# Kernel optimization log

Hardware: AMD Instinct MI355X
Metric: run time of the kernel (lower is better)

The kernel has to match this reference:

```python
import jax, jax.numpy as jnp
import numpy as np

N_Q, N_KV, DIM, D_K, D_V = 4096, 4096, 1024, 1024, 1024

def setup_inputs() -> dict:
    key = jax.random.key(0)
    ks = jax.random.split(key, 6)
    return {
        "q": jax.random.normal(ks[0], (N_Q, DIM), dtype=jnp.float32),
        "k": jax.random.normal(ks[1], (N_KV, DIM), dtype=jnp.float32),
        "v": jax.random.normal(ks[2], (N_KV, DIM), dtype=jnp.float32),
        "W_q": jax.random.uniform(ks[3], (DIM, D_K), dtype=jnp.float32),
        "W_k": jax.random.uniform(ks[4], (DIM, D_V), dtype=jnp.float32),
        "W_v": jax.random.uniform(ks[5], (DIM, D_V), dtype=jnp.float32),
    }

def reference(q, k, v, W_q, W_k, W_v) -> jnp.ndarray:
    d_k = W_q.shape[1]
    Q = q @ W_q                      # (n, d_k)
    K = k @ W_k                      # (N, d_v)
    V = v @ W_v                      # (N, d_v)
    scores = (Q @ K.T) / jnp.sqrt(jnp.asarray(d_k, Q.dtype))  # (n, N)
    attn = jax.nn.softmax(scores, axis=-1)
    return attn @ V                  # (n, d_v)
```

## Files before the change

kernel.cpp:

```cpp
#include <hip/hip_runtime.h>
#include <hip/hip_bf16.h>
#include <stdint.h>

typedef float  f32x4  __attribute__((ext_vector_type(4)));
typedef short  s16x8  __attribute__((ext_vector_type(8)));
typedef unsigned short u16;

#define BK 32

__device__ inline u16 f32_to_bf16_rn(float f) {
  uint32_t u = __builtin_bit_cast(uint32_t, f);
  u += 0x7FFFu + ((u >> 16) & 1u);
  return (u16)(u >> 16);
}
__device__ inline float bf16u_to_f32(u16 h) {
  uint32_t u = ((uint32_t)h) << 16;
  return __builtin_bit_cast(float, u);
}
__device__ inline void split2(float x, u16& hi, u16& lo) {
  u16 h = f32_to_bf16_rn(x);
  lo = f32_to_bf16_rn(x - bf16u_to_f32(h));
  hi = h;
}

__device__ inline void stage16(const u16* g, const u16* l) {
  __builtin_amdgcn_global_load_lds((const __attribute__((address_space(1))) uint32_t*)g,
                                   (__attribute__((address_space(3))) uint32_t*)(u16*)l,
                                   16, 0, 0);
}

__device__ inline void xcd_swz(int& bx, int& by) {
  int nx = gridDim.x, nwg = nx * gridDim.y;
  if ((nwg & 7) == 0) {
    int wg = blockIdx.x + nx * blockIdx.y;
    int s = (wg & 7) * (nwg >> 3) + (wg >> 3);
    bx = s % nx;
    by = s / nx;
  } else {
    bx = blockIdx.x;
    by = blockIdx.y;
  }
}


__global__ __launch_bounds__(256) void split_rows3(const float* __restrict__ in0,
                                                   const float* __restrict__ in1,
                                                   const float* __restrict__ in2,
                                                   u16* __restrict__ hi0, u16* __restrict__ lo0,
                                                   u16* __restrict__ hi1, u16* __restrict__ lo1,
                                                   u16* __restrict__ hi2, u16* __restrict__ lo2,
                                                   int n4) {
  int i = blockIdx.x * 256 + threadIdx.x;
  if (i >= n4) return;
  const float* in = blockIdx.z == 0 ? in0 : blockIdx.z == 1 ? in1 : in2;
  u16* hi = blockIdx.z == 0 ? hi0 : blockIdx.z == 1 ? hi1 : hi2;
  u16* lo = blockIdx.z == 0 ? lo0 : blockIdx.z == 1 ? lo1 : lo2;
  float4 t = ((const float4*)in)[i];
  ushort4 h, l;
  split2(t.x, h.x, l.x);
  split2(t.y, h.y, l.y);
  split2(t.z, h.z, l.z);
  split2(t.w, h.w, l.w);
  ((ushort4*)hi)[i] = h;
  ((ushort4*)lo)[i] = l;
}

__global__ __launch_bounds__(256) void split_transpose3(const float* __restrict__ in0,
                                                        const float* __restrict__ in1,
                                                        const float* __restrict__ in2,
                                                        u16* __restrict__ thi0, u16* __restrict__ tlo0,
                                                        u16* __restrict__ thi1, u16* __restrict__ tlo1,
                                                        u16* __restrict__ thi2, u16* __restrict__ tlo2,
                                                        int R, int C) {
  const float* in = blockIdx.z == 0 ? in0 : blockIdx.z == 1 ? in1 : in2;
  u16* thi = blockIdx.z == 0 ? thi0 : blockIdx.z == 1 ? thi1 : thi2;
  u16* tlo = blockIdx.z == 0 ? tlo0 : blockIdx.z == 1 ? tlo1 : tlo2;
  __shared__ float tile[32][33];
  int tx = threadIdx.x & 31, ty = threadIdx.x >> 5;
  int r0 = blockIdx.y * 32, c0 = blockIdx.x * 32;
#pragma unroll
  for (int j = 0; j < 32; j += 8)
    tile[ty + j][tx] = in[(size_t)(r0 + ty + j) * C + c0 + tx];
  __syncthreads();
#pragma unroll
  for (int j = 0; j < 32; j += 8) {
    float x = tile[tx][ty + j];
    u16 h, l;
    split2(x, h, l);
    size_t o = (size_t)(c0 + ty + j) * R + r0 + tx;
    thi[o] = h;
    tlo[o] = l;
  }
}

__global__ __launch_bounds__(256) void transpose_u16_2(const u16* __restrict__ in0,
                                                       const u16* __restrict__ in1,
                                                       u16* __restrict__ out0,
                                                       u16* __restrict__ out1, int R, int C) {
  const u16* in = blockIdx.z == 0 ? in0 : in1;
  u16* out = blockIdx.z == 0 ? out0 : out1;
  __shared__ u16 tile[32][33];
  int tx = threadIdx.x & 31, ty = threadIdx.x >> 5;
  int r0 = blockIdx.y * 32, c0 = blockIdx.x * 32;
#pragma unroll
  for (int j = 0; j < 32; j += 8)
    tile[ty + j][tx] = in[(size_t)(r0 + ty + j) * C + c0 + tx];
  __syncthreads();
#pragma unroll
  for (int j = 0; j < 32; j += 8)
    out[(size_t)(c0 + ty + j) * R + r0 + tx] = tile[tx][ty + j];
}

__global__ __launch_bounds__(256) void add_inplace(float* __restrict__ a,
                                                   const float* __restrict__ b, int n4) {
  int i = blockIdx.x * 256 + threadIdx.x;
  if (i >= n4) return;
  float4 x = ((const float4*)a)[i];
  float4 y = ((const float4*)b)[i];
  x.x += y.x; x.y += y.y; x.z += y.z; x.w += y.w;
  ((float4*)a)[i] = x;
}

template <int TBN, int OUT_SPLIT>
__device__ __forceinline__ void gemm8p_body(
    const u16* __restrict__ Ahi, const u16* __restrict__ Alo, int lda,
    const u16* __restrict__ Bhi, const u16* __restrict__ Blo, int ldb,
    float* __restrict__ Cf, u16* __restrict__ Chi, u16* __restrict__ Clo, int ldc,
    int NT, int k0, float scale, int arow0, int bcol0) {
  constexpr int NW = TBN / 4;
  constexpr int FN = NW / 16;
  constexpr int NCA = 256 * 8;
  constexpr int NCB = TBN * 8;
  constexpr int TISS = (NCA + NCB) / 512;
  constexpr int H1 = (TISS + 1) / 2;
  constexpr int BB = NCA * 8;

  __shared__ alignas(16) u16 lds[2][(NCA + NCB) * 8];

  const int tid = threadIdx.x;
  const int lane = tid & 63;
  const int wid = tid >> 6;
  const int wr = wid >> 2;
  const int wc = wid & 3;
  const int frow = lane & 15;
  const int koct = lane >> 4;

  const u16* src[TISS];
  int loff[TISS];
#pragma unroll
  for (int j = 0; j < TISS; ++j) {
    int g = j * 512 + wid * 64 + lane;
    loff[j] = g * 8;
    if (g < NCA) {
      int r = g >> 3, ch = g & 7, c2 = ch ^ (r & 7);
      const u16* base = (c2 < 4) ? Ahi : Alo;
      src[j] = base + (size_t)(arow0 + r) * lda + k0 + (c2 & 3) * 8;
    } else {
      int gb = g - NCA;
      int r = gb >> 3, ch = gb & 7, c2 = ch ^ (r & 7);
      const u16* base = (c2 < 4) ? Bhi : Blo;
      src[j] = base + (size_t)(bcol0 + r) * ldb + k0 + (c2 & 3) * 8;
    }
  }

  f32x4 acc[8][FN];
#pragma unroll
  for (int m = 0; m < 8; ++m)
#pragma unroll
    for (int n = 0; n < FN; ++n) acc[m][n] = (f32x4)0.0f;

#pragma unroll
  for (int j = 0; j < TISS; ++j) stage16(src[j], &lds[0][loff[j]]);
#pragma unroll
  for (int j = 0; j < TISS; ++j) src[j] += BK;
  asm volatile("s_waitcnt vmcnt(0)" ::: "memory");
  __builtin_amdgcn_sched_barrier(0);
  __builtin_amdgcn_s_barrier();

  for (int t = 0; t < NT; ++t) {
    const u16* cur = lds[t & 1];
    const u16* nxt = lds[(t + 1) & 1];
    const bool st = (t + 1 < NT);
    s16x8 bh[FN], bl[FN];
#pragma unroll
    for (int p = 0; p < 4; ++p) {
      s16x8 ah[2], al[2];
      if (p == 0) {
#pragma unroll
        for (int n = 0; n < FN; ++n) {
          int br = wc * NW + n * 16 + frow;
          bh[n] = *(const s16x8*)&cur[BB + br * 64 + ((koct ^ (br & 7)) << 3)];
          bl[n] = *(const s16x8*)&cur[BB + br * 64 + (((4 | koct) ^ (br & 7)) << 3)];
        }
      }
#pragma unroll
      for (int m = 0; m < 2; ++m) {
        int ar = wr * 128 + p * 32 + m * 16 + frow;
        ah[m] = *(const s16x8*)&cur[ar * 64 + ((koct ^ (ar & 7)) << 3)];
        al[m] = *(const s16x8*)&cur[ar * 64 + (((4 | koct) ^ (ar & 7)) << 3)];
      }
      if (st && p == 0) {
#pragma unroll
        for (int j = 0; j < H1; ++j) stage16(src[j], &nxt[loff[j]]);
      }
      if (st && p == 1) {
#pragma unroll
        for (int j = H1; j < TISS; ++j) stage16(src[j], &nxt[loff[j]]);
#pragma unroll
        for (int j = 0; j < TISS; ++j) src[j] += BK;
      }
      __builtin_amdgcn_sched_barrier(0);
      __builtin_amdgcn_s_barrier();
      asm volatile("s_waitcnt lgkmcnt(0)" ::: "memory");
      __builtin_amdgcn_sched_barrier(0);
      __builtin_amdgcn_s_setprio(1);
#pragma unroll
      for (int m = 0; m < 2; ++m)
#pragma unroll
        for (int n = 0; n < FN; ++n) {
          acc[p * 2 + m][n] =
              __builtin_amdgcn_mfma_f32_16x16x32_bf16(ah[m], bh[n], acc[p * 2 + m][n], 0, 0, 0);
          acc[p * 2 + m][n] =
              __builtin_amdgcn_mfma_f32_16x16x32_bf16(ah[m], bl[n], acc[p * 2 + m][n], 0, 0, 0);
          acc[p * 2 + m][n] =
              __builtin_amdgcn_mfma_f32_16x16x32_bf16(al[m], bh[n], acc[p * 2 + m][n], 0, 0, 0);
        }
      __builtin_amdgcn_s_setprio(0);
      __builtin_amdgcn_sched_barrier(0);
      if (p == 3) {
        asm volatile("s_waitcnt vmcnt(0)" ::: "memory");
        __builtin_amdgcn_sched_barrier(0);
      }
      __builtin_amdgcn_s_barrier();
    }
  }

  const int rb = arow0 + wr * 128 + koct * 4;
  const int cb = bcol0 + wc * NW + frow;
#pragma unroll
  for (int mg = 0; mg < 8; ++mg)
#pragma unroll
    for (int n = 0; n < FN; ++n)
#pragma unroll
      for (int r = 0; r < 4; ++r) {
        int row = rb + mg * 16 + r;
        int col = cb + n * 16;
        float val = acc[mg][n][r] * scale;
        if (OUT_SPLIT) {
          u16 h, l;
          split2(val, h, l);
          Chi[(size_t)row * ldc + col] = h;
          Clo[(size_t)row * ldc + col] = l;
        } else {
          Cf[(size_t)row * ldc + col] = val;
        }
      }
}

__global__ __launch_bounds__(512, 2) void scores8p(
    const u16* __restrict__ Ahi, const u16* __restrict__ Alo, int lda,
    const u16* __restrict__ Bhi, const u16* __restrict__ Blo, int ldb,
    float* __restrict__ Cf, int ldc, int NT, float scale) {
  int bx, by;
  xcd_swz(bx, by);
  gemm8p_body<256, 0>(Ahi, Alo, lda, Bhi, Blo, ldb, Cf, nullptr, nullptr, ldc,
                      NT, 0, scale, by * 256, bx * 256);
}

__global__ __launch_bounds__(512, 2) void proj8p(
    const u16* __restrict__ a0h, const u16* __restrict__ a0l,
    const u16* __restrict__ a1h, const u16* __restrict__ a1l,
    const u16* __restrict__ a2h, const u16* __restrict__ a2l,
    const u16* __restrict__ b0h, const u16* __restrict__ b0l,
    const u16* __restrict__ b1h, const u16* __restrict__ b1l,
    const u16* __restrict__ b2h, const u16* __restrict__ b2l,
    u16* __restrict__ c0h, u16* __restrict__ c0l,
    u16* __restrict__ c1h, u16* __restrict__ c1l,
    u16* __restrict__ c2h, u16* __restrict__ c2l,
    int D, float scale0) {
  const int z = blockIdx.z;
  const u16* Ah = z == 0 ? a0h : z == 1 ? a1h : a2h;
  const u16* Al = z == 0 ? a0l : z == 1 ? a1l : a2l;
  const u16* Bh = z == 0 ? b0h : z == 1 ? b1h : b2h;
  const u16* Bl = z == 0 ? b0l : z == 1 ? b1l : b2l;
  u16* Ch = z == 0 ? c0h : z == 1 ? c1h : c2h;
  u16* Cl = z == 0 ? c0l : z == 1 ? c1l : c2l;
  float scale = z == 0 ? scale0 : 1.0f;
  int bx, by;
  xcd_swz(bx, by);
  gemm8p_body<128, 1>(Ah, Al, D, Bh, Bl, D, nullptr, Ch, Cl, D,
                      D / BK, 0, scale, by * 256, bx * 128);
}

__global__ __launch_bounds__(512, 2) void pv8p(
    const u16* __restrict__ Ahi, const u16* __restrict__ Alo, int lda,
    const u16* __restrict__ Bhi, const u16* __restrict__ Blo, int ldb,
    float* __restrict__ Cf0, float* __restrict__ Cf1, int ldc, int KH) {
  float* Cf = blockIdx.z == 0 ? Cf0 : Cf1;
  int bx, by;
  xcd_swz(bx, by);
  gemm8p_body<128, 0>(Ahi, Alo, lda, Bhi, Blo, ldb, Cf, nullptr, nullptr, ldc,
                      KH / BK, blockIdx.z * KH, 1.0f, by * 256, bx * 128);
}

__global__ __launch_bounds__(256) void softmax_rows(float* __restrict__ S, int N) {
  const int tid = threadIdx.x;
  float* row = S + (size_t)blockIdx.x * N;
  const float4* row4 = (const float4*)row;
  float v[16];
#pragma unroll
  for (int i = 0; i < 4; ++i) {
    float4 t = row4[tid + i * 256];
    v[i * 4 + 0] = t.x;
    v[i * 4 + 1] = t.y;
    v[i * 4 + 2] = t.z;
    v[i * 4 + 3] = t.w;
  }
  float m = -__builtin_inff();
#pragma unroll
  for (int i = 0; i < 16; ++i) m = fmaxf(m, v[i]);
#pragma unroll
  for (int o = 32; o > 0; o >>= 1) m = fmaxf(m, __shfl_xor(m, o));
  __shared__ float redm[4];
  __shared__ float reds[4];
  const int wid = tid >> 6;
  if ((tid & 63) == 0) redm[wid] = m;
  __syncthreads();
  m = fmaxf(fmaxf(redm[0], redm[1]), fmaxf(redm[2], redm[3]));

  float s = 0.f;
#pragma unroll
  for (int i = 0; i < 16; ++i) {
    v[i] = __expf(v[i] - m);
    s += v[i];
  }
#pragma unroll
  for (int o = 32; o > 0; o >>= 1) s += __shfl_xor(s, o);
  if ((tid & 63) == 0) reds[wid] = s;
  __syncthreads();
  s = reds[0] + reds[1] + reds[2] + reds[3];
  float inv = 1.0f / s;

  u16* hrow = (u16*)row;
  u16* lrow = hrow + N;
#pragma unroll
  for (int i = 0; i < 4; ++i) {
    ushort4 h4, l4;
    split2(v[i * 4 + 0] * inv, h4.x, l4.x);
    split2(v[i * 4 + 1] * inv, h4.y, l4.y);
    split2(v[i * 4 + 2] * inv, h4.z, l4.z);
    split2(v[i * 4 + 3] * inv, h4.w, l4.w);
    ((ushort4*)hrow)[tid + i * 256] = h4;
    ((ushort4*)lrow)[tid + i * 256] = l4;
  }
}

extern "C" void kernel_launch(void* const* d_in, const int* in_sizes, int n_in,
                              void* d_out, int out_size, void* d_ws, size_t ws_size,
                              hipStream_t stream) {
  (void)in_sizes; (void)n_in; (void)out_size; (void)ws_size;
  const float* q  = (const float*)d_in[0];
  const float* k  = (const float*)d_in[1];
  const float* v  = (const float*)d_in[2];
  const float* Wq = (const float*)d_in[3];
  const float* Wk = (const float*)d_in[4];
  const float* Wv = (const float*)d_in[5];
  float* out = (float*)d_out;

  char* ws = (char*)d_ws;
  const size_t MB = 1ull << 20;
  u16* q_hi = (u16*)(ws + 0 * MB);
  u16* q_lo = (u16*)(ws + 8 * MB);
  u16* k_hi = (u16*)(ws + 16 * MB);
  u16* k_lo = (u16*)(ws + 24 * MB);
  u16* v_hi = (u16*)(ws + 32 * MB);
  u16* v_lo = (u16*)(ws + 40 * MB);
  u16* V_hi = (u16*)(ws + 48 * MB);
  u16* V_lo = (u16*)(ws + 56 * MB);
  float* S  = (float*)(ws + 0 * MB);
  u16* WqT_hi = (u16*)(ws + 64 * MB);
  u16* WqT_lo = (u16*)(ws + 66 * MB);
  u16* WkT_hi = (u16*)(ws + 68 * MB);
  u16* WkT_lo = (u16*)(ws + 70 * MB);
  u16* WvT_hi = (u16*)(ws + 72 * MB);
  u16* WvT_lo = (u16*)(ws + 74 * MB);
  u16* Q_hi = (u16*)(ws + 76 * MB);
  u16* Q_lo = (u16*)(ws + 84 * MB);
  u16* K_hi = (u16*)(ws + 92 * MB);
  u16* K_lo = (u16*)(ws + 100 * MB);
  u16* VT_hi = (u16*)(ws + 108 * MB);
  u16* VT_lo = (u16*)(ws + 116 * MB);
  float* PVp1 = (float*)(ws + 76 * MB);

  const int NQ = 4096, NKV = 4096, D = 1024;

  int n4 = NQ * D / 4;
  split_rows3<<<dim3(n4 / 256, 1, 3), 256, 0, stream>>>(q, k, v, q_hi, q_lo, k_hi, k_lo,
                                                        v_hi, v_lo, n4);

  split_transpose3<<<dim3(D / 32, D / 32, 3), 256, 0, stream>>>(
      Wq, Wk, Wv, WqT_hi, WqT_lo, WkT_hi, WkT_lo, WvT_hi, WvT_lo, D, D);

  proj8p<<<dim3(D / 128, NQ / 256, 3), 512, 0, stream>>>(
      q_hi, q_lo, k_hi, k_lo, v_hi, v_lo,
      WqT_hi, WqT_lo, WkT_hi, WkT_lo, WvT_hi, WvT_lo,
      Q_hi, Q_lo, K_hi, K_lo, V_hi, V_lo, D, 0.03125f);

  transpose_u16_2<<<dim3(D / 32, NKV / 32, 2), 256, 0, stream>>>(V_hi, V_lo, VT_hi, VT_lo,
                                                                 NKV, D);

  scores8p<<<dim3(NKV / 256, NQ / 256), 512, 0, stream>>>(Q_hi, Q_lo, D, K_hi, K_lo, D,
                                                          S, NKV, D / BK, 1.0f);

  softmax_rows<<<NQ, 256, 0, stream>>>(S, NKV);

  pv8p<<<dim3(D / 128, NQ / 256, 2), 512, 0, stream>>>(
      (u16*)S, (u16*)S + NKV, 2 * NKV, VT_hi, VT_lo, NKV, out, PVp1, D, NKV / 2);

  add_inplace<<<NQ * D / 4 / 256, 256, 0, stream>>>(out, PVp1, NQ * D / 4);
}
```

Baseline: 405.5 us.

## Triple-buffer GEMM LDS pipeline and shrink scores tile to 256x128

The shared GEMM body goes from double to triple buffering in LDS, prefetching two K-steps ahead and using partial vmcnt waits so global loads overlap more compute. The scores kernel also drops from 256x256 to 256x128 tiles, doubling its grid, and the body is fixed at a 128-wide N tile. Three 48KB buffers raise LDS use to 144KB per block, which may cut the two-blocks-per-CU occupancy the launch bounds request. The scores tile change lowers operand reuse per block.

```diff
diff --git a/kernel.cpp b/kernel.cpp
--- a/kernel.cpp
+++ b/kernel.cpp
@@ -121,21 +121,20 @@
   ((float4*)a)[i] = x;
 }
 
-template <int TBN, int OUT_SPLIT>
-__device__ __forceinline__ void gemm8p_body(
+template <int OUT_SPLIT>
+__device__ __forceinline__ void gemm3b_body(
     const u16* __restrict__ Ahi, const u16* __restrict__ Alo, int lda,
     const u16* __restrict__ Bhi, const u16* __restrict__ Blo, int ldb,
     float* __restrict__ Cf, u16* __restrict__ Chi, u16* __restrict__ Clo, int ldc,
     int NT, int k0, float scale, int arow0, int bcol0) {
-  constexpr int NW = TBN / 4;
-  constexpr int FN = NW / 16;
   constexpr int NCA = 256 * 8;
-  constexpr int NCB = TBN * 8;
+  constexpr int NCB = 128 * 8;
   constexpr int TISS = (NCA + NCB) / 512;
-  constexpr int H1 = (TISS + 1) / 2;
+  constexpr int H1 = TISS / 2;
   constexpr int BB = NCA * 8;
-
-  __shared__ alignas(16) u16 lds[2][(NCA + NCB) * 8];
+  constexpr int BUFSZ = (NCA + NCB) * 8;
+
+  __shared__ alignas(16) u16 lds[3][BUFSZ];
 
   const int tid = threadIdx.x;
   const int lane = tid & 63;
@@ -163,32 +162,40 @@
     }
   }
 
-  f32x4 acc[8][FN];
+  f32x4 acc[8][2];
 #pragma unroll
   for (int m = 0; m < 8; ++m)
 #pragma unroll
-    for (int n = 0; n < FN; ++n) acc[m][n] = (f32x4)0.0f;
+    for (int n = 0; n < 2; ++n) acc[m][n] = (f32x4)0.0f;
 
 #pragma unroll
   for (int j = 0; j < TISS; ++j) stage16(src[j], &lds[0][loff[j]]);
 #pragma unroll
   for (int j = 0; j < TISS; ++j) src[j] += BK;
-  asm volatile("s_waitcnt vmcnt(0)" ::: "memory");
+  if (NT > 1) {
+#pragma unroll
+    for (int j = 0; j < TISS; ++j) stage16(src[j], &lds[1][loff[j]]);
+#pragma unroll
+    for (int j = 0; j < TISS; ++j) src[j] += BK;
+    asm volatile("s_waitcnt vmcnt(6)" ::: "memory");
+  } else {
+    asm volatile("s_waitcnt vmcnt(0)" ::: "memory");
+  }
   __builtin_amdgcn_sched_barrier(0);
   __builtin_amdgcn_s_barrier();
 
   for (int t = 0; t < NT; ++t) {
-    const u16* cur = lds[t & 1];
-    const u16* nxt = lds[(t + 1) & 1];
-    const bool st = (t + 1 < NT);
-    s16x8 bh[FN], bl[FN];
+    const u16* cur = lds[t % 3];
+    const u16* nx2 = lds[(t + 2) % 3];
+    const bool st = (t + 2 < NT);
+    s16x8 bh[2], bl[2];
 #pragma unroll
     for (int p = 0; p < 4; ++p) {
       s16x8 ah[2], al[2];
       if (p == 0) {
 #pragma unroll
-        for (int n = 0; n < FN; ++n) {
-          int br = wc * NW + n * 16 + frow;
+        for (int n = 0; n < 2; ++n) {
+          int br = wc * 32 + n * 16 + frow;
           bh[n] = *(const s16x8*)&cur[BB + br * 64 + ((koct ^ (br & 7)) << 3)];
           bl[n] = *(const s16x8*)&cur[BB + br * 64 + (((4 | koct) ^ (br & 7)) << 3)];
         }
@@ -201,11 +208,11 @@
       }
       if (st && p == 0) {
 #pragma unroll
-        for (int j = 0; j < H1; ++j) stage16(src[j], &nxt[loff[j]]);
+        for (int j = 0; j < H1; ++j) stage16(src[j], &nx2[loff[j]]);
       }
       if (st && p == 1) {
 #pragma unroll
-        for (int j = H1; j < TISS; ++j) stage16(src[j], &nxt[loff[j]]);
+        for (int j = H1; j < TISS; ++j) stage16(src[j], &nx2[loff[j]]);
 #pragma unroll
         for (int j = 0; j < TISS; ++j) src[j] += BK;
       }
@@ -217,7 +224,7 @@
 #pragma unroll
       for (int m = 0; m < 2; ++m)
 #pragma unroll
-        for (int n = 0; n < FN; ++n) {
+        for (int n = 0; n < 2; ++n) {
           acc[p * 2 + m][n] =
               __builtin_amdgcn_mfma_f32_16x16x32_bf16(ah[m], bh[n], acc[p * 2 + m][n], 0, 0, 0);
           acc[p * 2 + m][n] =
@@ -228,7 +235,11 @@
       __builtin_amdgcn_s_setprio(0);
       __builtin_amdgcn_sched_barrier(0);
       if (p == 3) {
-        asm volatile("s_waitcnt vmcnt(0)" ::: "memory");
+        if (st) {
+          asm volatile("s_waitcnt vmcnt(6)" ::: "memory");
+        } else {
+          asm volatile("s_waitcnt vmcnt(0)" ::: "memory");
+        }
         __builtin_amdgcn_sched_barrier(0);
       }
       __builtin_amdgcn_s_barrier();
@@ -236,11 +247,11 @@
   }
 
   const int rb = arow0 + wr * 128 + koct * 4;
-  const int cb = bcol0 + wc * NW + frow;
+  const int cb = bcol0 + wc * 32 + frow;
 #pragma unroll
   for (int mg = 0; mg < 8; ++mg)
 #pragma unroll
-    for (int n = 0; n < FN; ++n)
+    for (int n = 0; n < 2; ++n)
 #pragma unroll
       for (int r = 0; r < 4; ++r) {
         int row = rb + mg * 16 + r;
@@ -263,8 +274,8 @@
     float* __restrict__ Cf, int ldc, int NT, float scale) {
   int bx, by;
   xcd_swz(bx, by);
-  gemm8p_body<256, 0>(Ahi, Alo, lda, Bhi, Blo, ldb, Cf, nullptr, nullptr, ldc,
-                      NT, 0, scale, by * 256, bx * 256);
+  gemm3b_body<0>(Ahi, Alo, lda, Bhi, Blo, ldb, Cf, nullptr, nullptr, ldc,
+                 NT, 0, scale, by * 256, bx * 128);
 }
 
 __global__ __launch_bounds__(512, 2) void proj8p(
@@ -288,8 +299,8 @@
   float scale = z == 0 ? scale0 : 1.0f;
   int bx, by;
   xcd_swz(bx, by);
-  gemm8p_body<128, 1>(Ah, Al, D, Bh, Bl, D, nullptr, Ch, Cl, D,
-                      D / BK, 0, scale, by * 256, bx * 128);
+  gemm3b_body<1>(Ah, Al, D, Bh, Bl, D, nullptr, Ch, Cl, D,
+                 D / BK, 0, scale, by * 256, bx * 128);
 }
 
 __global__ __launch_bounds__(512, 2) void pv8p(
@@ -299,8 +310,8 @@
   float* Cf = blockIdx.z == 0 ? Cf0 : Cf1;
   int bx, by;
   xcd_swz(bx, by);
-  gemm8p_body<128, 0>(Ahi, Alo, lda, Bhi, Blo, ldb, Cf, nullptr, nullptr, ldc,
-                      KH / BK, blockIdx.z * KH, 1.0f, by * 256, bx * 128);
+  gemm3b_body<0>(Ahi, Alo, lda, Bhi, Blo, ldb, Cf, nullptr, nullptr, ldc,
+                 KH / BK, blockIdx.z * KH, 1.0f, by * 256, bx * 128);
 }
 
 __global__ __launch_bounds__(256) void softmax_rows(float* __restrict__ S, int N) {
@@ -409,7 +420,7 @@
   transpose_u16_2<<<dim3(D / 32, NKV / 32, 2), 256, 0, stream>>>(V_hi, V_lo, VT_hi, VT_lo,
                                                                  NKV, D);
 
-  scores8p<<<dim3(NKV / 256, NQ / 256), 512, 0, stream>>>(Q_hi, Q_lo, D, K_hi, K_lo, D,
+  scores8p<<<dim3(NKV / 128, NQ / 256), 512, 0, stream>>>(Q_hi, Q_lo, D, K_hi, K_lo, D,
                                                           S, NKV, D / BK, 1.0f);
 
   softmax_rows<<<NQ, 256, 0, stream>>>(S, NKV);
```

After: 431.7 us. 6.5% more time.

## Reorder GEMM tile staging for partial vmcnt waits and widen projection tiles

Applied to the files above, without the earlier changes.

The shared GEMM body now issues the B-tile loads first and then the A-tile loads in an interleaved order. It replaces the full vmcnt(0) drain with partial waits at phases 1 and 3, so the next tile's global loads can keep flowing while the current data is consumed. The projection kernel also moves from 256x128 to 256x256 tiles, which halves its grid and raises reuse per block but adds register pressure and cuts parallelism. The partial-wait counts rely on the exact order of issued loads, which adds a correctness risk.

```diff
diff --git a/kernel.cpp b/kernel.cpp
--- a/kernel.cpp
+++ b/kernel.cpp
@@ -122,17 +122,16 @@
 }
 
 template <int TBN, int OUT_SPLIT>
-__device__ __forceinline__ void gemm8p_body(
+__device__ __forceinline__ void gemm2c_body(
     const u16* __restrict__ Ahi, const u16* __restrict__ Alo, int lda,
     const u16* __restrict__ Bhi, const u16* __restrict__ Blo, int ldb,
     float* __restrict__ Cf, u16* __restrict__ Chi, u16* __restrict__ Clo, int ldc,
     int NT, int k0, float scale, int arow0, int bcol0) {
-  constexpr int NW = TBN / 4;
-  constexpr int FN = NW / 16;
-  constexpr int NCA = 256 * 8;
+  constexpr int NCA = 2048;
   constexpr int NCB = TBN * 8;
-  constexpr int TISS = (NCA + NCB) / 512;
-  constexpr int H1 = (TISS + 1) / 2;
+  constexpr int NBI = NCB / 512;
+  constexpr int TISS = NBI + 4;
+  constexpr int FN = TBN / 64;
   constexpr int BB = NCA * 8;
 
   __shared__ alignas(16) u16 lds[2][(NCA + NCB) * 8];
@@ -147,19 +146,21 @@
 
   const u16* src[TISS];
   int loff[TISS];
-#pragma unroll
-  for (int j = 0; j < TISS; ++j) {
-    int g = j * 512 + wid * 64 + lane;
-    loff[j] = g * 8;
-    if (g < NCA) {
+  const int aj[4] = {0, 2, 1, 3};
+#pragma unroll
+  for (int s = 0; s < TISS; ++s) {
+    if (s < NBI) {
+      int g = s * 512 + tid;
+      int r = g >> 3, ch = g & 7, c2 = ch ^ (r & 7);
+      const u16* base = (c2 < 4) ? Bhi : Blo;
+      src[s] = base + (size_t)(bcol0 + r) * ldb + k0 + (c2 & 3) * 8;
+      loff[s] = BB + g * 8;
+    } else {
+      int g = aj[s - NBI] * 512 + tid;
       int r = g >> 3, ch = g & 7, c2 = ch ^ (r & 7);
       const u16* base = (c2 < 4) ? Ahi : Alo;
-      src[j] = base + (size_t)(arow0 + r) * lda + k0 + (c2 & 3) * 8;
-    } else {
-      int gb = g - NCA;
-      int r = gb >> 3, ch = gb & 7, c2 = ch ^ (r & 7);
-      const u16* base = (c2 < 4) ? Bhi : Blo;
-      src[j] = base + (size_t)(bcol0 + r) * ldb + k0 + (c2 & 3) * 8;
+      src[s] = base + (size_t)(arow0 + r) * lda + k0 + (c2 & 3) * 8;
+      loff[s] = g * 8;
     }
   }
 
@@ -170,10 +171,10 @@
     for (int n = 0; n < FN; ++n) acc[m][n] = (f32x4)0.0f;
 
 #pragma unroll
-  for (int j = 0; j < TISS; ++j) stage16(src[j], &lds[0][loff[j]]);
-#pragma unroll
-  for (int j = 0; j < TISS; ++j) src[j] += BK;
-  asm volatile("s_waitcnt vmcnt(0)" ::: "memory");
+  for (int s = 0; s < TISS; ++s) stage16(src[s], &lds[0][loff[s]]);
+#pragma unroll
+  for (int s = 0; s < TISS; ++s) src[s] += BK;
+  asm volatile("s_waitcnt vmcnt(2)" ::: "memory");
   __builtin_amdgcn_sched_barrier(0);
   __builtin_amdgcn_s_barrier();
 
@@ -188,7 +189,7 @@
       if (p == 0) {
 #pragma unroll
         for (int n = 0; n < FN; ++n) {
-          int br = wc * NW + n * 16 + frow;
+          int br = wc * (TBN / 4) + n * 16 + frow;
           bh[n] = *(const s16x8*)&cur[BB + br * 64 + ((koct ^ (br & 7)) << 3)];
           bl[n] = *(const s16x8*)&cur[BB + br * 64 + (((4 | koct) ^ (br & 7)) << 3)];
         }
@@ -201,13 +202,13 @@
       }
       if (st && p == 0) {
 #pragma unroll
-        for (int j = 0; j < H1; ++j) stage16(src[j], &nxt[loff[j]]);
+        for (int s = 0; s < TISS - 2; ++s) stage16(src[s], &nxt[loff[s]]);
       }
       if (st && p == 1) {
 #pragma unroll
-        for (int j = H1; j < TISS; ++j) stage16(src[j], &nxt[loff[j]]);
-#pragma unroll
-        for (int j = 0; j < TISS; ++j) src[j] += BK;
+        for (int s = TISS - 2; s < TISS; ++s) stage16(src[s], &nxt[loff[s]]);
+#pragma unroll
+        for (int s = 0; s < TISS; ++s) src[s] += BK;
       }
       __builtin_amdgcn_sched_barrier(0);
       __builtin_amdgcn_s_barrier();
@@ -227,8 +228,16 @@
         }
       __builtin_amdgcn_s_setprio(0);
       __builtin_amdgcn_sched_barrier(0);
-      if (p == 3) {
-        asm volatile("s_waitcnt vmcnt(0)" ::: "memory");
+      if (p == 1) {
+        if (st) {
+          asm volatile("s_waitcnt vmcnt(%0)" ::"i"(TISS) : "memory");
+        } else {
+          asm volatile("s_waitcnt vmcnt(0)" ::: "memory");
+        }
+        __builtin_amdgcn_sched_barrier(0);
+      }
+      if (p == 3 && st) {
+        asm volatile("s_waitcnt vmcnt(2)" ::: "memory");
         __builtin_amdgcn_sched_barrier(0);
       }
       __builtin_amdgcn_s_barrier();
@@ -236,7 +245,7 @@
   }
 
   const int rb = arow0 + wr * 128 + koct * 4;
-  const int cb = bcol0 + wc * NW + frow;
+  const int cb = bcol0 + wc * (TBN / 4) + frow;
 #pragma unroll
   for (int mg = 0; mg < 8; ++mg)
 #pragma unroll
@@ -263,7 +272,7 @@
     float* __restrict__ Cf, int ldc, int NT, float scale) {
   int bx, by;
   xcd_swz(bx, by);
-  gemm8p_body<256, 0>(Ahi, Alo, lda, Bhi, Blo, ldb, Cf, nullptr, nullptr, ldc,
+  gemm2c_body<256, 0>(Ahi, Alo, lda, Bhi, Blo, ldb, Cf, nullptr, nullptr, ldc,
                       NT, 0, scale, by * 256, bx * 256);
 }
 
@@ -288,8 +297,8 @@
   float scale = z == 0 ? scale0 : 1.0f;
   int bx, by;
   xcd_swz(bx, by);
-  gemm8p_body<128, 1>(Ah, Al, D, Bh, Bl, D, nullptr, Ch, Cl, D,
-                      D / BK, 0, scale, by * 256, bx * 128);
+  gemm2c_body<256, 1>(Ah, Al, D, Bh, Bl, D, nullptr, Ch, Cl, D,
+                      D / BK, 0, scale, by * 256, bx * 256);
 }
 
 __global__ __launch_bounds__(512, 2) void pv8p(
@@ -299,7 +308,7 @@
   float* Cf = blockIdx.z == 0 ? Cf0 : Cf1;
   int bx, by;
   xcd_swz(bx, by);
-  gemm8p_body<128, 0>(Ahi, Alo, lda, Bhi, Blo, ldb, Cf, nullptr, nullptr, ldc,
+  gemm2c_body<128, 0>(Ahi, Alo, lda, Bhi, Blo, ldb, Cf, nullptr, nullptr, ldc,
                       KH / BK, blockIdx.z * KH, 1.0f, by * 256, bx * 128);
 }
 
@@ -401,7 +410,7 @@
   split_transpose3<<<dim3(D / 32, D / 32, 3), 256, 0, stream>>>(
       Wq, Wk, Wv, WqT_hi, WqT_lo, WkT_hi, WkT_lo, WvT_hi, WvT_lo, D, D);
 
-  proj8p<<<dim3(D / 128, NQ / 256, 3), 512, 0, stream>>>(
+  proj8p<<<dim3(D / 256, NQ / 256, 3), 512, 0, stream>>>(
       q_hi, q_lo, k_hi, k_lo, v_hi, v_lo,
       WqT_hi, WqT_lo, WkT_hi, WkT_lo, WvT_hi, WvT_lo,
       Q_hi, Q_lo, K_hi, K_lo, V_hi, V_lo, D, 0.03125f);
```

After: 399.0 us. No clear change (-1.6%).
